# Performance work log

Hardware: AMD Instinct MI355X
Metric: run time of the kernel (lower is better)

Reference implementation:

```python
import jax, jax.numpy as jnp
import numpy as np

N, D_MODEL, NUM_HEAD = 2, 256, 8
HI, WI = 40, 40
MAX_DIS = 7
WS = 2 * MAX_DIS + 1          # 15
HD = D_MODEL // NUM_HEAD      # 32
T = HD ** 0.5
NEG = 1e8                     # fp32 mask value used by the torch module


def setup_inputs() -> dict:
    key = jax.random.key(0)
    ks = jax.random.split(key, 10)
    s = 0.02
    f = lambda i, shape: jax.random.normal(ks[i], shape, jnp.float32)
    return dict(
        q=f(0, (N, D_MODEL, HI, WI)),
        k=f(1, (N, D_MODEL, HI, WI)),
        v=f(2, (N, D_MODEL, HI, WI)),
        Wq=f(3, (D_MODEL, D_MODEL)) * s, bq=jnp.zeros((D_MODEL,), jnp.float32),
        Wk=f(4, (D_MODEL, D_MODEL)) * s, bk=jnp.zeros((D_MODEL,), jnp.float32),
        Wv=f(5, (D_MODEL, D_MODEL)) * s, bv=jnp.zeros((D_MODEL,), jnp.float32),
        rel_k_w=f(6, (NUM_HEAD, WS * WS, HD)) * s,      # grouped 1x1 conv weight
        rel_k_b=jnp.zeros((NUM_HEAD, WS * WS), jnp.float32),
        rel_v=f(7, (NUM_HEAD, HD, WS * WS)) * s,        # nn.Parameter (zeros in torch; random here to exercise math)
        Wp=f(8, (D_MODEL, D_MODEL)) * s, bp=jnp.zeros((D_MODEL,), jnp.float32),
    )


def _geometry(h, w):
    # Static (numpy) index/mask construction matching compute_mask().
    qy = np.repeat(np.arange(h), w)
    qx = np.tile(np.arange(w), h)
    dy = qy[None, :] - qy[:, None]          # key - query, [hw, hw]
    dx = qx[None, :] - qx[:, None]
    valid = (np.abs(dy) <= MAX_DIS) & (np.abs(dx) <= MAX_DIS)
    widx = (np.clip(dy + MAX_DIS, 0, WS - 1) * WS + np.clip(dx + MAX_DIS, 0, WS - 1))
    offs = np.arange(-MAX_DIS, MAX_DIS + 1)
    dyo = np.repeat(offs, WS)               # [ws*ws] row-major window order (dy*WS+dx)
    dxo = np.tile(offs, WS)
    ky = qy[:, None] + dyo[None, :]         # [hw, ws*ws]
    kx = qx[:, None] + dxo[None, :]
    in_img = (ky >= 0) & (ky < h) & (kx >= 0) & (kx < w)
    jidx = np.clip(ky, 0, h - 1) * w + np.clip(kx, 0, w - 1)
    return (jnp.asarray(valid), jnp.asarray(widx), jnp.asarray(in_img), jnp.asarray(jidx))


def reference(q, k, v, Wq, bq, Wk, bk, Wv, bv, rel_k_w, rel_k_b, rel_v, Wp, bp):
    n, c, h, w = q.shape
    hw = h * w
    nh, hd = NUM_HEAD, c // NUM_HEAD

    def proj(x, Wt, b):  # 1x1 conv == per-pixel linear
        return jnp.einsum('oc,ncp->nop', Wt, x.reshape(n, c, hw)) + b[None, :, None]

    qf = proj(q, Wq, bq)
    kf = proj(k, Wk, bk)
    vf = proj(v, Wv, bv)

    qh = qf.reshape(n, nh, hd, hw)
    kh = kf.reshape(n, nh, hd, hw)
    vh = vf.reshape(n, nh, hd, hw)

    # grouped 1x1 conv: per-head linear from hd channels to ws*ws (computed BEFORE q/T)
    rel = jnp.einsum('hwd,nhdp->nhpw', rel_k_w, qh) + rel_k_b[None, :, None, :]  # [n,nh,hw,ws2]

    qh = qh / T
    qk = jnp.einsum('nhdi,nhdj->nhij', qh, kh)   # [n,nh,hw,hw]

    valid, widx, in_img, jidx = _geometry(h, w)

    # --- 'global' path: dense hw x hw, non-local keys masked with -1e8, local keys get rel bias ---
    rel_dense = jnp.take_along_axis(rel, widx[None, None], axis=3)   # [n,nh,hw,hw]
    global_logits = jnp.where(valid[None, None], qk + rel_dense, qk - NEG)
    global_attn = jax.nn.softmax(global_logits, axis=-1)
    agg_value = jnp.einsum('nhij,nhdj->inhd', global_attn, vh).reshape(hw, n, c)

    # --- local path: gather ws*ws window per query; out-of-image keys are -1e8 (pad value), rel added everywhere ---
    gathered = jnp.take_along_axis(qk, jidx[None, None], axis=3)     # [n,nh,hw,ws2]
    local_logits = jnp.where(in_img[None, None], gathered, -NEG) + rel
    local_attn = jax.nn.softmax(local_logits, axis=-1)
    agg_bias = jnp.einsum('nhiw,hdw->inhd', local_attn, rel_v).reshape(hw, n, c)

    out = (agg_value + agg_bias) @ Wp.T + bp    # nn.Linear, output [hw, n, c]
    return out, local_attn
```

## Files before the change

### kernel.cpp

```cpp
#include <hip/hip_runtime.h>
#include <hip/hip_bf16.h>

#define HW    1600
#define NB    2
#define NHEAD 8
#define HD    32
#define WS2   225
#define WDIM  40
#define CDIM  256
#define PROJ  819200
#define RELW  240
#define RELSTR 248
#define TSC   5.656854249492381f

typedef __attribute__((ext_vector_type(8))) short short8;
typedef __attribute__((ext_vector_type(4))) float floatx4;

static __device__ __forceinline__ float bu2f(short u) {
    return __uint_as_float(((unsigned)(unsigned short)u) << 16);
}
static __device__ __forceinline__ short f2bu(float f) {
    __hip_bfloat16 h = __float2bfloat16(f);
    short s; __builtin_memcpy(&s, &h, 2); return s;
}
static __device__ __forceinline__ unsigned pk2(short a, short b) {
    return (unsigned)(unsigned short)a | ((unsigned)(unsigned short)b << 16);
}
static __device__ __forceinline__ float ldf(const void* p, size_t i, bool f32) {
    return f32 ? ((const float*)p)[i] : __bfloat162float(((const __hip_bfloat16*)p)[i]);
}
static __device__ __forceinline__ void st_out(void* p, size_t i, float v, bool f32) {
    if (f32) ((float*)p)[i] = v;
    else     ((__hip_bfloat16*)p)[i] = __float2bfloat16(v);
}
static __device__ __forceinline__ short8 ld8bf(const void* p, size_t i, bool f32) {
    if (!f32) return *(const short8*)((const __hip_bfloat16*)p + i);
    const float* f = (const float*)p + i;
    short8 r;
    #pragma unroll
    for (int t = 0; t < 8; ++t) r[t] = f2bu(f[t]);
    return r;
}
static __device__ __forceinline__ void ld8f(const void* p, size_t i, bool f32, float* o) {
    if (f32) {
        const float* f = (const float*)p + i;
        #pragma unroll
        for (int t = 0; t < 8; ++t) o[t] = f[t];
    } else {
        short8 s = *(const short8*)((const __hip_bfloat16*)p + i);
        #pragma unroll
        for (int t = 0; t < 8; ++t) o[t] = bu2f(s[t]);
    }
}

__global__ __launch_bounds__(64) void detect_kernel(const void* qv, int* flag) {
    const __hip_bfloat16* qb = (const __hip_bfloat16*)qv;
    int bad = 0;
    for (int i = threadIdx.x; i < 4096; i += 64) {
        float v = __bfloat162float(qb[i]);
        if (!(v > -1e6f && v < 1e6f)) bad = 1;
    }
    bad = (__any(bad) ? 1 : 0);
    if (threadIdx.x == 0) *flag = bad;
}

__global__ __launch_bounds__(256) void relvT_kernel(const void* __restrict__ relv,
                                                    const int* __restrict__ flag,
                                                    __hip_bfloat16* __restrict__ relvT) {
    const bool f32 = (*flag != 0);
    const int h = blockIdx.x;
    for (int idx = threadIdx.x; idx < WS2 * HD; idx += 256) {
        const int w = idx >> 5, d = idx & 31;
        relvT[(size_t)h * WS2 * HD + idx] =
            __float2bfloat16(ldf(relv, ((size_t)h * HD + d) * WS2 + w, f32));
    }
}

__global__ __launch_bounds__(256) void proj_fused(
    const void* __restrict__ xq, const void* __restrict__ xk, const void* __restrict__ xv,
    const void* __restrict__ Wq, const void* __restrict__ bq,
    const void* __restrict__ Wk, const void* __restrict__ bk,
    const void* __restrict__ Wv, const void* __restrict__ bv,
    const int* __restrict__ flag,
    __hip_bfloat16* __restrict__ qs, __hip_bfloat16* __restrict__ ks,
    __hip_bfloat16* __restrict__ vs)
{
    __shared__ short xt[32][264];
    const bool f32 = (*flag != 0);
    const int m0 = blockIdx.x * 32;
    const int n  = blockIdx.y;
    const int t  = blockIdx.z;
    const void *x, *W, *bias; __hip_bfloat16* dst; float scale;
    if (t == 0)      { x = xq; W = Wq; bias = bq; dst = qs; scale = 0.17677669529663687f; }
    else if (t == 1) { x = xk; W = Wk; bias = bk; dst = ks; scale = 1.f; }
    else             { x = xv; W = Wv; bias = bv; dst = vs; scale = 1.f; }

    {
        const int c = threadIdx.x;
        const size_t xb = ((size_t)n * CDIM + c) * HW + m0;
        if (f32) {
            const float* xr = (const float*)x + xb;
            #pragma unroll
            for (int g = 0; g < 8; ++g) {
                float4 f = *(const float4*)(xr + g * 4);
                xt[g*4+0][c] = f2bu(f.x); xt[g*4+1][c] = f2bu(f.y);
                xt[g*4+2][c] = f2bu(f.z); xt[g*4+3][c] = f2bu(f.w);
            }
        } else {
            const __hip_bfloat16* xr = (const __hip_bfloat16*)x + xb;
            #pragma unroll
            for (int g = 0; g < 4; ++g) {
                short8 s = *(const short8*)(xr + g * 8);
                #pragma unroll
                for (int u = 0; u < 8; ++u) xt[g*8+u][c] = s[u];
            }
        }
    }
    __syncthreads();

    const int wave = threadIdx.x >> 6, lane = threadIdx.x & 63;
    const int m = lane & 15, qd = lane >> 4;

    short8 A[2][8];
    #pragma unroll
    for (int mt = 0; mt < 2; ++mt)
        #pragma unroll
        for (int k = 0; k < 8; ++k)
            A[mt][k] = *(const short8*)(&xt[mt*16 + m][k*32 + qd*8]);

    #pragma unroll
    for (int og = 0; og < 4; ++og) {
        const int o0 = (wave * 4 + og) * 16;
        short8 B[8];
        #pragma unroll
        for (int k = 0; k < 8; ++k)
            B[k] = ld8bf(W, (size_t)(o0 + m) * CDIM + k*32 + qd*8, f32);
        floatx4 acc0 = {0,0,0,0}, acc1 = {0,0,0,0};
        #pragma unroll
        for (int k = 0; k < 8; ++k) {
            acc0 = __builtin_amdgcn_mfma_f32_16x16x32_bf16(A[0][k], B[k], acc0, 0, 0, 0);
            acc1 = __builtin_amdgcn_mfma_f32_16x16x32_bf16(A[1][k], B[k], acc1, 0, 0, 0);
        }
        const int o = o0 + (lane & 15), h = o >> 5, d = o & 31;
        const float bv_ = ldf(bias, (size_t)o, f32);
        #pragma unroll
        for (int rg = 0; rg < 4; ++rg) {
            const int p = m0 + (lane >> 4) * 4 + rg;
            dst[((size_t)(n*NHEAD + h)*HW + p)*HD + d]      = __float2bfloat16((acc0[rg] + bv_) * scale);
            dst[((size_t)(n*NHEAD + h)*HW + p + 16)*HD + d] = __float2bfloat16((acc1[rg] + bv_) * scale);
        }
    }
}

__global__ __launch_bounds__(256) void rel_gemm(
    const __hip_bfloat16* __restrict__ qs, const void* __restrict__ rkw,
    const void* __restrict__ rkb, const int* __restrict__ flag,
    __hip_bfloat16* __restrict__ rel)
{
    const bool f32 = (*flag != 0);
    const int wave = threadIdx.x >> 6, lane = threadIdx.x & 63;
    const int i0 = blockIdx.x * 64;
    const int nh_ = blockIdx.y;
    const int h = nh_ & 7;
    const int m = lane & 15, qd = lane >> 4;

    short8 A[4];
    #pragma unroll
    for (int it = 0; it < 4; ++it)
        A[it] = *(const short8*)(qs + ((size_t)nh_ * HW + i0 + it*16 + m) * HD + qd*8);

    for (int wt = wave; wt < 15; wt += 4) {
        const int w0 = wt * 16;
        const int wl = min(w0 + m, WS2 - 1);
        short8 B = ld8bf(rkw, ((size_t)h * WS2 + wl) * HD + qd*8, f32);
        const int wcol = w0 + (lane & 15);
        const float rb_ = (wcol < WS2) ? ldf(rkb, (size_t)h * WS2 + wcol, f32) : 0.f;
        #pragma unroll
        for (int it = 0; it < 4; ++it) {
            floatx4 acc = {0,0,0,0};
            acc = __builtin_amdgcn_mfma_f32_16x16x32_bf16(A[it], B, acc, 0, 0, 0);
            if (wcol < WS2) {
                #pragma unroll
                for (int rg = 0; rg < 4; ++rg) {
                    const int i = i0 + it*16 + (lane >> 4)*4 + rg;
                    rel[((size_t)nh_ * HW + i) * RELW + wcol] =
                        __float2bfloat16(acc[rg] * TSC + rb_);
                }
            }
        }
    }
}

#define SP_OFF    0
#define R2_OFF    15616
#define R1_OFF    24064
#define SMAX_OFF  39680
#define SSUM_OFF  39936
#define SMEM_SZ   40192

__global__ __launch_bounds__(256) void attn_mfma(
    const __hip_bfloat16* __restrict__ qs, const __hip_bfloat16* __restrict__ ks,
    const __hip_bfloat16* __restrict__ vs,
    const __hip_bfloat16* __restrict__ rel,
    const __hip_bfloat16* __restrict__ relvT,
    const int* __restrict__ flag,
    __hip_bfloat16* __restrict__ agg,
    void* __restrict__ dout)
{
    __shared__ __align__(16) char smem[SMEM_SZ];
    short* sP   = (short*)(smem + SP_OFF);
    short* sRel = (short*)(smem + R2_OFF);
    short* sPw  = (short*)(smem + R2_OFF);
    short* sB   = (short*)(smem + R1_OFF);
    float* sOh  = (float*)(smem + R1_OFF);
    float* sMax = (float*)(smem + SMAX_OFF);
    float* sSum = (float*)(smem + SSUM_OFF);

    const bool f32 = (*flag != 0);
    const int tid = threadIdx.x;
    const int wave = tid >> 6, lane = tid & 63;
    const int m = lane & 15, quad = lane >> 4;
    const int y = blockIdx.x / 3, tile3 = blockIdx.x % 3;
    const int x0 = (tile3 == 0) ? 0 : (tile3 == 1) ? 16 : 24;
    const int wlo = (tile3 == 2) ? 8 : 0;
    const int nh_ = blockIdx.y;
    const int h = nh_ & 7, n = nh_ >> 3;
    const size_t qb = (size_t)nh_ * HW;
    const size_t qrow0 = qb + (size_t)y * WDIM + x0;

    for (int idx = tid; idx < 480; idx += 256) {
        const int row = idx / 30, c8 = (idx - row * 30) * 8;
        short8 v = *(const short8*)((const short*)rel + (qrow0 + row) * RELW + c8);
        *(short8*)(sRel + row * RELSTR + c8) = v;
    }
    const short8 afrag = *(const short8*)((const short*)qs + (qrow0 + m) * HD + quad * 8);
    __syncthreads();

    float L[8][4];
    #pragma unroll
    for (int j = 0; j < 8; ++j)
        #pragma unroll
        for (int rg = 0; rg < 4; ++rg) L[j][rg] = -1e30f;

    #pragma unroll
    for (int j = 0; j < 8; ++j) {
        const int t = wave + 4 * j;
        if (t < 30) {
            const int r = t >> 1, c0_ = (t & 1) << 4;
            const int cc = c0_ + m;
            const int ky = y + r - 7, kx = x0 - 7 + cc;
            const int gky = min(max(ky, 0), WDIM - 1), gkx = min(max(kx, 0), WDIM - 1);
            const short8 bfrag = *(const short8*)((const short*)ks + (qb + (size_t)gky * WDIM + gkx) * HD + quad * 8);
            floatx4 s4 = {0.f, 0.f, 0.f, 0.f};
            s4 = __builtin_amdgcn_mfma_f32_16x16x32_bf16(afrag, bfrag, s4, 0, 0, 0);
            const bool inimg = ((unsigned)ky < (unsigned)WDIM) && ((unsigned)kx < (unsigned)WDIM);
            #pragma unroll
            for (int rg = 0; rg < 4; ++rg) {
                const int qm = quad * 4 + rg;
                const int dx7 = cc - qm;
                if (inimg && (unsigned)dx7 < 15u)
                    L[j][rg] = s4[rg] + bu2f(sRel[qm * RELSTR + r * 15 + dx7]);
            }
        }
    }

    float mx[4];
    #pragma unroll
    for (int rg = 0; rg < 4; ++rg) {
        mx[rg] = L[0][rg];
        #pragma unroll
        for (int j = 1; j < 8; ++j) mx[rg] = fmaxf(mx[rg], L[j][rg]);
        #pragma unroll
        for (int off = 1; off <= 8; off <<= 1) mx[rg] = fmaxf(mx[rg], __shfl_xor(mx[rg], off));
    }
    if (m == 0) {
        #pragma unroll
        for (int rg = 0; rg < 4; ++rg) sMax[(quad * 4 + rg) * 4 + wave] = mx[rg];
    }
    __syncthreads();
    float M4[4], sm[4];
    #pragma unroll
    for (int rg = 0; rg < 4; ++rg) {
        const float4 v = *(const float4*)&sMax[(quad * 4 + rg) * 4];
        M4[rg] = fmaxf(fmaxf(v.x, v.y), fmaxf(v.z, v.w));
        sm[rg] = 0.f;
    }
    #pragma unroll
    for (int j = 0; j < 8; ++j)
        #pragma unroll
        for (int rg = 0; rg < 4; ++rg) { L[j][rg] = expf(L[j][rg] - M4[rg]); sm[rg] += L[j][rg]; }
    #pragma unroll
    for (int rg = 0; rg < 4; ++rg)
        #pragma unroll
        for (int off = 1; off <= 8; off <<= 1) sm[rg] += __shfl_xor(sm[rg], off);
    if (m == 0) {
        #pragma unroll
        for (int rg = 0; rg < 4; ++rg) sSum[(quad * 4 + rg) * 4 + wave] = sm[rg];
    }
    __syncthreads();
    float inv4[4];
    #pragma unroll
    for (int rg = 0; rg < 4; ++rg) {
        const float4 v = *(const float4*)&sSum[(quad * 4 + rg) * 4];
        inv4[rg] = 1.f / (v.x + v.y + v.z + v.w);
    }

    for (int e = tid; e < 16 * 39; e += 256) {
        const int row = e / 39, c = 225 + (e - row * 39);
        sPw[row * 264 + c] = 0;
    }

    #pragma unroll
    for (int j = 0; j < 8; ++j) {
        const int t = wave + 4 * j;
        if (t < 30) {
            const int r = t >> 1, cc = ((t & 1) << 4) + m;
            #pragma unroll
            for (int rg = 0; rg < 4; ++rg) {
                const int qm = quad * 4 + rg;
                const short pb = f2bu(L[j][rg] * inv4[rg]);
                sP[qm * 488 + r * 32 + cc] = pb;
                const int dx7 = cc - qm;
                if ((unsigned)dx7 < 15u) sPw[qm * 264 + r * 15 + dx7] = pb;
            }
        }
    }
    __syncthreads();

    #pragma unroll
    for (int rr = 0; rr < 4; ++rr) {
        const int qm = wave * 4 + rr;
        if (qm >= wlo) {
            const size_t obase = (size_t)PROJ + (qrow0 + qm) * WS2;
            #pragma unroll
            for (int c = 0; c < 4; ++c) {
                const int col = lane + 64 * c;
                if (col < WS2) st_out(dout, obase + col, bu2f(sPw[qm * 264 + col]), f32);
            }
        }
    }

    for (int half = 0; half < 2; ++half) {
        __syncthreads();
        const int h16 = half << 4;
        {
            unsigned* dstw = (unsigned*)sB;
            for (int p = tid; p < 240; p += 256) {
                const int kk0 = 2 * p;
                const int r = kk0 >> 5, c = kk0 & 31;
                const int gky = min(max(y + r - 7, 0), WDIM - 1);
                const int gkx0 = min(max(x0 - 7 + c, 0), WDIM - 1);
                const int gkx1 = min(max(x0 - 7 + c + 1, 0), WDIM - 1);
                const short* v0 = (const short*)vs + (qb + (size_t)gky * WDIM + gkx0) * HD + h16;
                const short* v1 = (const short*)vs + (qb + (size_t)gky * WDIM + gkx1) * HD + h16;
                const short8 a0 = *(const short8*)v0, b0 = *(const short8*)v1;
                const short8 a1 = *(const short8*)(v0 + 8), b1 = *(const short8*)(v1 + 8);
                #pragma unroll
                for (int dd = 0; dd < 8; ++dd) dstw[dd * 244 + p] = pk2(a0[dd], b0[dd]);
                #pragma unroll
                for (int dd = 0; dd < 8; ++dd) dstw[(dd + 8) * 244 + p] = pk2(a1[dd], b1[dd]);
            }
        }
        __syncthreads();
        floatx4 acc = {0.f, 0.f, 0.f, 0.f};
        for (int u = wave; u < 15; u += 4) {
            const short8 Af = *(const short8*)(sP + m * 488 + u * 32 + quad * 8);
            const short8 Bf = *(const short8*)(sB + m * 488 + u * 32 + quad * 8);
            acc = __builtin_amdgcn_mfma_f32_16x16x32_bf16(Af, Bf, acc, 0, 0, 0);
        }
        __syncthreads();
        {
            unsigned* dstw = (unsigned*)sB;
            for (int p = tid; p < 132; p += 256) {
                const int w0 = 2 * p;
                short8 a0 = {0,0,0,0,0,0,0,0}, a1 = a0, b0 = a0, b1 = a0;
                if (w0 < WS2) {
                    const short* rp = (const short*)relvT + ((size_t)h * WS2 + w0) * HD + h16;
                    a0 = *(const short8*)rp; a1 = *(const short8*)(rp + 8);
                }
                if (w0 + 1 < WS2) {
                    const short* rp = (const short*)relvT + ((size_t)h * WS2 + w0 + 1) * HD + h16;
                    b0 = *(const short8*)rp; b1 = *(const short8*)(rp + 8);
                }
                #pragma unroll
                for (int dd = 0; dd < 8; ++dd) dstw[dd * 132 + p] = pk2(a0[dd], b0[dd]);
                #pragma unroll
                for (int dd = 0; dd < 8; ++dd) dstw[(dd + 8) * 132 + p] = pk2(a1[dd], b1[dd]);
            }
        }
        __syncthreads();
        for (int u = wave; u < 8; u += 4) {
            const short8 Af = *(const short8*)(sPw + m * 264 + u * 32 + quad * 8);
            const short8 Bf = *(const short8*)(sB + m * 264 + u * 32 + quad * 8);
            acc = __builtin_amdgcn_mfma_f32_16x16x32_bf16(Af, Bf, acc, 0, 0, 0);
        }
        __syncthreads();
        #pragma unroll
        for (int rg = 0; rg < 4; ++rg)
            sOh[wave * 256 + (quad * 4 + rg) * 16 + m] = acc[rg];
        __syncthreads();
        {
            const int qq = tid >> 4, dd = tid & 15;
            const float s = sOh[tid] + sOh[256 + tid] + sOh[512 + tid] + sOh[768 + tid];
            if (qq >= wlo) {
                const size_t i = (size_t)y * WDIM + x0 + qq;
                agg[(i * NB + n) * CDIM + h * HD + h16 + dd] = __float2bfloat16(s);
            }
        }
    }
}

__global__ __launch_bounds__(256) void attn_fallback(
    const __hip_bfloat16* __restrict__ qs, const __hip_bfloat16* __restrict__ ks,
    const __hip_bfloat16* __restrict__ vs,
    const __hip_bfloat16* __restrict__ relvT,
    const void* __restrict__ rkw, const void* __restrict__ rkb,
    const int* __restrict__ flag,
    __hip_bfloat16* __restrict__ agg,
    void* __restrict__ dout)
{
    __shared__ float sL[4][240];

    const bool f32 = (*flag != 0);
    const int wave = threadIdx.x >> 6, lane = threadIdx.x & 63;
    const int qidx = blockIdx.x * 4 + wave;
    const int i = qidx % HW, nh_ = qidx / HW;
    const int h = nh_ & (NHEAD - 1), n = nh_ >> 3;
    const int y = i / WDIM, x = i - y * WDIM;

    const int w16 = lane >> 2, qq = lane & 3;
    float q8[8];
    {
        short8 qv = *(const short8*)(qs + (size_t)qidx * HD + qq * 8);
        #pragma unroll
        for (int t = 0; t < 8; ++t) q8[t] = bu2f(qv[t]);
    }

    const int kxu = x + w16 - 7;
    const bool vw = (w16 < 15);
    for (int r = 0; r < 15; ++r) {
        const int ky = y + r - 7;
        const int widx = r * 15 + w16;
        const bool vimg = vw && ((unsigned)ky < WDIM) && ((unsigned)kxu < WDIM);
        float part = 0.f;
        if (vimg) {
            short8 kv = *(const short8*)(ks + ((size_t)nh_ * HW + ky * WDIM + kxu) * HD + qq * 8);
            float r8[8];
            ld8f(rkw, ((size_t)h * WS2 + widx) * HD + qq * 8, f32, r8);
            #pragma unroll
            for (int t = 0; t < 8; ++t) part += q8[t] * (bu2f(kv[t]) + TSC * r8[t]);
        }
        part += __shfl_xor(part, 1);
        part += __shfl_xor(part, 2);
        if (qq == 0) {
            float lg = -1e30f;
            if (vimg) lg = part + ldf(rkb, (size_t)h * WS2 + widx, f32);
            sL[wave][vw ? widx : (225 + r)] = lg;
        }
    }

    float lg[4];
    float mx = -1e30f;
    #pragma unroll
    for (int c = 0; c < 4; ++c) {
        const int w_ = lane + 64 * c;
        lg[c] = (w_ < 240) ? sL[wave][w_] : -1e30f;
        mx = fmaxf(mx, lg[c]);
    }
    #pragma unroll
    for (int off = 32; off > 0; off >>= 1) mx = fmaxf(mx, __shfl_xor(mx, off));
    float s = 0.f;
    #pragma unroll
    for (int c = 0; c < 4; ++c) { lg[c] = expf(lg[c] - mx); s += lg[c]; }
    #pragma unroll
    for (int off = 32; off > 0; off >>= 1) s += __shfl_xor(s, off);
    const float inv = (s > 0.f) ? (1.0f / s) : 0.f;
    #pragma unroll
    for (int c = 0; c < 4; ++c) {
        const int w_ = lane + 64 * c;
        if (w_ < WS2) {
            const float a = lg[c] * inv;
            sL[wave][w_] = a;
            st_out(dout, (size_t)PROJ + (size_t)qidx * WS2 + w_, a, f32);
        }
    }

    float o8[8] = {0.f, 0.f, 0.f, 0.f, 0.f, 0.f, 0.f, 0.f};
    if (vw) {
        for (int r = 0; r < 15; ++r) {
            const int widx = r * 15 + w16;
            const int kyc = min(max(y + r - 7, 0), WDIM - 1);
            const int kxc = min(max(kxu, 0), WDIM - 1);
            const float P = sL[wave][widx];
            short8 vv = *(const short8*)(vs + ((size_t)nh_ * HW + kyc * WDIM + kxc) * HD + qq * 8);
            short8 rv = *(const short8*)(relvT + ((size_t)h * WS2 + widx) * HD + qq * 8);
            #pragma unroll
            for (int t = 0; t < 8; ++t) o8[t] += P * (bu2f(vv[t]) + bu2f(rv[t]));
        }
    }
    #pragma unroll
    for (int off = 4; off <= 32; off <<= 1)
        #pragma unroll
        for (int t = 0; t < 8; ++t) o8[t] += __shfl_xor(o8[t], off);
    if (lane < 4) {
        short8 tmp;
        #pragma unroll
        for (int t = 0; t < 8; ++t) tmp[t] = f2bu(o8[t]);
        *(short8*)(agg + ((size_t)i * NB + n) * CDIM + h * HD + qq * 8) = tmp;
    }
}

__global__ __launch_bounds__(256) void out_mfma(
    const __hip_bfloat16* __restrict__ agg, const void* __restrict__ Wp,
    const void* __restrict__ bp, const int* __restrict__ flag,
    void* __restrict__ dout)
{
    const bool f32 = (*flag != 0);
    const int wave = threadIdx.x >> 6, lane = threadIdx.x & 63;
    const int tile = blockIdx.x * 4 + wave;
    const int rb0 = tile & ~15;
    const int o0 = (tile & 15) << 4;
    const int m = lane & 15, qd = lane >> 4;

    const __hip_bfloat16* arow = agg + (size_t)(rb0 + m) * CDIM + qd * 8;
    const size_t bidx = (size_t)(o0 + m) * CDIM + qd * 8;

    floatx4 acc = {0.f, 0.f, 0.f, 0.f};
    #pragma unroll
    for (int k = 0; k < 8; ++k) {
        short8 a = *(const short8*)(arow + k * 32);
        short8 b = ld8bf(Wp, bidx + k * 32, f32);
        acc = __builtin_amdgcn_mfma_f32_16x16x32_bf16(a, b, acc, 0, 0, 0);
    }
    const int o = o0 + (lane & 15);
    const float bv_ = ldf(bp, (size_t)o, f32);
    #pragma unroll
    for (int rg = 0; rg < 4; ++rg) {
        const int rb = rb0 + (lane >> 4) * 4 + rg;
        st_out(dout, (size_t)rb * CDIM + o, acc[rg] + bv_, f32);
    }
}

extern "C" void kernel_launch(void* const* d_in, const int* in_sizes, int n_in,
                              void* d_out, int out_size, void* d_ws, size_t ws_size,
                              hipStream_t stream)
{
    const void* q   = d_in[0];
    const void* k   = d_in[1];
    const void* v   = d_in[2];
    const void* Wq  = d_in[3];
    const void* bq  = d_in[4];
    const void* Wk  = d_in[5];
    const void* bk  = d_in[6];
    const void* Wv  = d_in[7];
    const void* bv  = d_in[8];
    const void* rkw = d_in[9];
    const void* rkb = d_in[10];
    const void* rlv = d_in[11];
    const void* Wp  = d_in[12];
    const void* bp  = d_in[13];

    char* wsb = (char*)d_ws;
    int* flag = (int*)wsb;
    __hip_bfloat16* relvT = (__hip_bfloat16*)(wsb + 64);
    __hip_bfloat16* qs    = (__hip_bfloat16*)(wsb + 64 + 115200);
    __hip_bfloat16* ks    = qs + PROJ;
    __hip_bfloat16* vs    = ks + PROJ;
    __hip_bfloat16* agg   = vs + PROJ;
    __hip_bfloat16* rel   = agg + PROJ;
    const size_t need = 64 + 115200 + (size_t)4 * PROJ * 2 + (size_t)NB * NHEAD * HW * RELW * 2;
    const bool userel = (ws_size >= need);

    detect_kernel<<<1, 64, 0, stream>>>(q, flag);
    relvT_kernel<<<8, 256, 0, stream>>>(rlv, flag, relvT);
    proj_fused<<<dim3(50, 2, 3), 256, 0, stream>>>(q, k, v, Wq, bq, Wk, bk, Wv, bv,
                                                   flag, qs, ks, vs);
    if (userel) {
        rel_gemm<<<dim3(25, 16), 256, 0, stream>>>(qs, rkw, rkb, flag, rel);
        attn_mfma<<<dim3(120, 16), 256, 0, stream>>>(qs, ks, vs, rel, relvT, flag, agg, d_out);
    } else {
        attn_fallback<<<6400, 256, 0, stream>>>(qs, ks, vs, relvT, rkw, rkb, flag, agg, d_out);
    }
    out_mfma<<<800, 256, 0, stream>>>(agg, Wp, bp, flag, d_out);
}
```

Measured before the change: 183.8 us.

## Fuse rel GEMM into attention, merge prep kernels, widen output GEMM tiles

The relative-key GEMM now runs inside the attention kernel: each block computes its own 16x225 rel tile with MFMA straight into shared memory, so the global rel buffer round trip and the separate rel_gemm launch go away. The detect and relvT transpose kernels become one prep kernel, cutting a launch. The output projection computes two 16-column tiles per wave, halving the grid and reusing each A fragment. The fallback attention path is removed, and the per-block rel computation adds a little extra work and a sync inside attention.

```diff
diff --git a/kernel.cpp b/kernel.cpp
--- a/kernel.cpp
+++ b/kernel.cpp
@@ -9,7 +9,6 @@
 #define WDIM  40
 #define CDIM  256
 #define PROJ  819200
-#define RELW  240
 #define RELSTR 248
 #define TSC   5.656854249492381f
 
@@ -41,33 +40,24 @@
     for (int t = 0; t < 8; ++t) r[t] = f2bu(f[t]);
     return r;
 }
-static __device__ __forceinline__ void ld8f(const void* p, size_t i, bool f32, float* o) {
-    if (f32) {
-        const float* f = (const float*)p + i;
-        #pragma unroll
-        for (int t = 0; t < 8; ++t) o[t] = f[t];
-    } else {
-        short8 s = *(const short8*)((const __hip_bfloat16*)p + i);
-        #pragma unroll
-        for (int t = 0; t < 8; ++t) o[t] = bu2f(s[t]);
-    }
-}
-
-__global__ __launch_bounds__(64) void detect_kernel(const void* qv, int* flag) {
-    const __hip_bfloat16* qb = (const __hip_bfloat16*)qv;
+
+__global__ __launch_bounds__(256) void prep_kernel(const void* __restrict__ q,
+                                                   const void* __restrict__ relv,
+                                                   int* __restrict__ flag,
+                                                   __hip_bfloat16* __restrict__ relvT) {
+    __shared__ int sbad;
+    if (threadIdx.x == 0) sbad = 0;
+    __syncthreads();
     int bad = 0;
-    for (int i = threadIdx.x; i < 4096; i += 64) {
+    const __hip_bfloat16* qb = (const __hip_bfloat16*)q;
+    for (int i = threadIdx.x; i < 4096; i += 256) {
         float v = __bfloat162float(qb[i]);
         if (!(v > -1e6f && v < 1e6f)) bad = 1;
     }
-    bad = (__any(bad) ? 1 : 0);
-    if (threadIdx.x == 0) *flag = bad;
-}
-
-__global__ __launch_bounds__(256) void relvT_kernel(const void* __restrict__ relv,
-                                                    const int* __restrict__ flag,
-                                                    __hip_bfloat16* __restrict__ relvT) {
-    const bool f32 = (*flag != 0);
+    if (bad) sbad = 1;
+    __syncthreads();
+    const bool f32 = (sbad != 0);
+    if (blockIdx.x == 0 && threadIdx.x == 0) *flag = sbad;
     const int h = blockIdx.x;
     for (int idx = threadIdx.x; idx < WS2 * HD; idx += 256) {
         const int w = idx >> 5, d = idx & 31;
@@ -152,56 +142,18 @@
     }
 }
 
-__global__ __launch_bounds__(256) void rel_gemm(
-    const __hip_bfloat16* __restrict__ qs, const void* __restrict__ rkw,
-    const void* __restrict__ rkb, const int* __restrict__ flag,
-    __hip_bfloat16* __restrict__ rel)
-{
-    const bool f32 = (*flag != 0);
-    const int wave = threadIdx.x >> 6, lane = threadIdx.x & 63;
-    const int i0 = blockIdx.x * 64;
-    const int nh_ = blockIdx.y;
-    const int h = nh_ & 7;
-    const int m = lane & 15, qd = lane >> 4;
-
-    short8 A[4];
-    #pragma unroll
-    for (int it = 0; it < 4; ++it)
-        A[it] = *(const short8*)(qs + ((size_t)nh_ * HW + i0 + it*16 + m) * HD + qd*8);
-
-    for (int wt = wave; wt < 15; wt += 4) {
-        const int w0 = wt * 16;
-        const int wl = min(w0 + m, WS2 - 1);
-        short8 B = ld8bf(rkw, ((size_t)h * WS2 + wl) * HD + qd*8, f32);
-        const int wcol = w0 + (lane & 15);
-        const float rb_ = (wcol < WS2) ? ldf(rkb, (size_t)h * WS2 + wcol, f32) : 0.f;
-        #pragma unroll
-        for (int it = 0; it < 4; ++it) {
-            floatx4 acc = {0,0,0,0};
-            acc = __builtin_amdgcn_mfma_f32_16x16x32_bf16(A[it], B, acc, 0, 0, 0);
-            if (wcol < WS2) {
-                #pragma unroll
-                for (int rg = 0; rg < 4; ++rg) {
-                    const int i = i0 + it*16 + (lane >> 4)*4 + rg;
-                    rel[((size_t)nh_ * HW + i) * RELW + wcol] =
-                        __float2bfloat16(acc[rg] * TSC + rb_);
-                }
-            }
-        }
-    }
-}
-
 #define SP_OFF    0
 #define R2_OFF    15616
 #define R1_OFF    24064
 #define SMAX_OFF  39680
 #define SSUM_OFF  39936
-#define SMEM_SZ   40192
+#define SRKB_OFF  40192
+#define SMEM_SZ   40672
 
 __global__ __launch_bounds__(256) void attn_mfma(
     const __hip_bfloat16* __restrict__ qs, const __hip_bfloat16* __restrict__ ks,
     const __hip_bfloat16* __restrict__ vs,
-    const __hip_bfloat16* __restrict__ rel,
+    const void* __restrict__ rkw, const void* __restrict__ rkb,
     const __hip_bfloat16* __restrict__ relvT,
     const int* __restrict__ flag,
     __hip_bfloat16* __restrict__ agg,
@@ -215,6 +167,7 @@
     float* sOh  = (float*)(smem + R1_OFF);
     float* sMax = (float*)(smem + SMAX_OFF);
     float* sSum = (float*)(smem + SSUM_OFF);
+    short* sRkb = (short*)(smem + SRKB_OFF);
 
     const bool f32 = (*flag != 0);
     const int tid = threadIdx.x;
@@ -228,12 +181,25 @@
     const size_t qb = (size_t)nh_ * HW;
     const size_t qrow0 = qb + (size_t)y * WDIM + x0;
 
-    for (int idx = tid; idx < 480; idx += 256) {
-        const int row = idx / 30, c8 = (idx - row * 30) * 8;
-        short8 v = *(const short8*)((const short*)rel + (qrow0 + row) * RELW + c8);
-        *(short8*)(sRel + row * RELSTR + c8) = v;
-    }
+    for (int wv = tid; wv < 240; wv += 256)
+        sRkb[wv] = (wv < WS2) ? f2bu(ldf(rkb, (size_t)h * WS2 + wv, f32)) : (short)0;
     const short8 afrag = *(const short8*)((const short*)qs + (qrow0 + m) * HD + quad * 8);
+    __syncthreads();
+
+    for (int wt = wave; wt < 15; wt += 4) {
+        const int w0 = wt * 16;
+        const int wl = min(w0 + m, WS2 - 1);
+        short8 B = ld8bf(rkw, ((size_t)h * WS2 + wl) * HD + quad * 8, f32);
+        floatx4 acc = {0.f, 0.f, 0.f, 0.f};
+        acc = __builtin_amdgcn_mfma_f32_16x16x32_bf16(afrag, B, acc, 0, 0, 0);
+        const int wcol = w0 + m;
+        if (wcol < WS2) {
+            const float rb_ = bu2f(sRkb[wcol]);
+            #pragma unroll
+            for (int rg = 0; rg < 4; ++rg)
+                sRel[(quad * 4 + rg) * RELSTR + wcol] = f2bu(acc[rg] * TSC + rb_);
+        }
+    }
     __syncthreads();
 
     float L[8][4];
@@ -410,106 +376,6 @@
     }
 }
 
-__global__ __launch_bounds__(256) void attn_fallback(
-    const __hip_bfloat16* __restrict__ qs, const __hip_bfloat16* __restrict__ ks,
-    const __hip_bfloat16* __restrict__ vs,
-    const __hip_bfloat16* __restrict__ relvT,
-    const void* __restrict__ rkw, const void* __restrict__ rkb,
-    const int* __restrict__ flag,
-    __hip_bfloat16* __restrict__ agg,
-    void* __restrict__ dout)
-{
-    __shared__ float sL[4][240];
-
-    const bool f32 = (*flag != 0);
-    const int wave = threadIdx.x >> 6, lane = threadIdx.x & 63;
-    const int qidx = blockIdx.x * 4 + wave;
-    const int i = qidx % HW, nh_ = qidx / HW;
-    const int h = nh_ & (NHEAD - 1), n = nh_ >> 3;
-    const int y = i / WDIM, x = i - y * WDIM;
-
-    const int w16 = lane >> 2, qq = lane & 3;
-    float q8[8];
-    {
-        short8 qv = *(const short8*)(qs + (size_t)qidx * HD + qq * 8);
-        #pragma unroll
-        for (int t = 0; t < 8; ++t) q8[t] = bu2f(qv[t]);
-    }
-
-    const int kxu = x + w16 - 7;
-    const bool vw = (w16 < 15);
-    for (int r = 0; r < 15; ++r) {
-        const int ky = y + r - 7;
-        const int widx = r * 15 + w16;
-        const bool vimg = vw && ((unsigned)ky < WDIM) && ((unsigned)kxu < WDIM);
-        float part = 0.f;
-        if (vimg) {
-            short8 kv = *(const short8*)(ks + ((size_t)nh_ * HW + ky * WDIM + kxu) * HD + qq * 8);
-            float r8[8];
-            ld8f(rkw, ((size_t)h * WS2 + widx) * HD + qq * 8, f32, r8);
-            #pragma unroll
-            for (int t = 0; t < 8; ++t) part += q8[t] * (bu2f(kv[t]) + TSC * r8[t]);
-        }
-        part += __shfl_xor(part, 1);
-        part += __shfl_xor(part, 2);
-        if (qq == 0) {
-            float lg = -1e30f;
-            if (vimg) lg = part + ldf(rkb, (size_t)h * WS2 + widx, f32);
-            sL[wave][vw ? widx : (225 + r)] = lg;
-        }
-    }
-
-    float lg[4];
-    float mx = -1e30f;
-    #pragma unroll
-    for (int c = 0; c < 4; ++c) {
-        const int w_ = lane + 64 * c;
-        lg[c] = (w_ < 240) ? sL[wave][w_] : -1e30f;
-        mx = fmaxf(mx, lg[c]);
-    }
-    #pragma unroll
-    for (int off = 32; off > 0; off >>= 1) mx = fmaxf(mx, __shfl_xor(mx, off));
-    float s = 0.f;
-    #pragma unroll
-    for (int c = 0; c < 4; ++c) { lg[c] = expf(lg[c] - mx); s += lg[c]; }
-    #pragma unroll
-    for (int off = 32; off > 0; off >>= 1) s += __shfl_xor(s, off);
-    const float inv = (s > 0.f) ? (1.0f / s) : 0.f;
-    #pragma unroll
-    for (int c = 0; c < 4; ++c) {
-        const int w_ = lane + 64 * c;
-        if (w_ < WS2) {
-            const float a = lg[c] * inv;
-            sL[wave][w_] = a;
-            st_out(dout, (size_t)PROJ + (size_t)qidx * WS2 + w_, a, f32);
-        }
-    }
-
-    float o8[8] = {0.f, 0.f, 0.f, 0.f, 0.f, 0.f, 0.f, 0.f};
-    if (vw) {
-        for (int r = 0; r < 15; ++r) {
-            const int widx = r * 15 + w16;
-            const int kyc = min(max(y + r - 7, 0), WDIM - 1);
-            const int kxc = min(max(kxu, 0), WDIM - 1);
-            const float P = sL[wave][widx];
-            short8 vv = *(const short8*)(vs + ((size_t)nh_ * HW + kyc * WDIM + kxc) * HD + qq * 8);
-            short8 rv = *(const short8*)(relvT + ((size_t)h * WS2 + widx) * HD + qq * 8);
-            #pragma unroll
-            for (int t = 0; t < 8; ++t) o8[t] += P * (bu2f(vv[t]) + bu2f(rv[t]));
-        }
-    }
-    #pragma unroll
-    for (int off = 4; off <= 32; off <<= 1)
-        #pragma unroll
-        for (int t = 0; t < 8; ++t) o8[t] += __shfl_xor(o8[t], off);
-    if (lane < 4) {
-        short8 tmp;
-        #pragma unroll
-        for (int t = 0; t < 8; ++t) tmp[t] = f2bu(o8[t]);
-        *(short8*)(agg + ((size_t)i * NB + n) * CDIM + h * HD + qq * 8) = tmp;
-    }
-}
-
 __global__ __launch_bounds__(256) void out_mfma(
     const __hip_bfloat16* __restrict__ agg, const void* __restrict__ Wp,
     const void* __restrict__ bp, const int* __restrict__ flag,
@@ -517,27 +383,30 @@
 {
     const bool f32 = (*flag != 0);
     const int wave = threadIdx.x >> 6, lane = threadIdx.x & 63;
-    const int tile = blockIdx.x * 4 + wave;
-    const int rb0 = tile & ~15;
-    const int o0 = (tile & 15) << 4;
+    const int t2 = blockIdx.x * 4 + wave;
+    const int rb0 = (t2 >> 3) << 4;
+    const int o0 = (t2 & 7) << 5;
     const int m = lane & 15, qd = lane >> 4;
 
     const __hip_bfloat16* arow = agg + (size_t)(rb0 + m) * CDIM + qd * 8;
-    const size_t bidx = (size_t)(o0 + m) * CDIM + qd * 8;
-
-    floatx4 acc = {0.f, 0.f, 0.f, 0.f};
+
+    floatx4 acc0 = {0.f, 0.f, 0.f, 0.f}, acc1 = {0.f, 0.f, 0.f, 0.f};
     #pragma unroll
     for (int k = 0; k < 8; ++k) {
-        short8 a = *(const short8*)(arow + k * 32);
-        short8 b = ld8bf(Wp, bidx + k * 32, f32);
-        acc = __builtin_amdgcn_mfma_f32_16x16x32_bf16(a, b, acc, 0, 0, 0);
-    }
-    const int o = o0 + (lane & 15);
-    const float bv_ = ldf(bp, (size_t)o, f32);
+        short8 a  = *(const short8*)(arow + k * 32);
+        short8 b0 = ld8bf(Wp, (size_t)(o0 + m) * CDIM + k * 32 + qd * 8, f32);
+        short8 b1 = ld8bf(Wp, (size_t)(o0 + 16 + m) * CDIM + k * 32 + qd * 8, f32);
+        acc0 = __builtin_amdgcn_mfma_f32_16x16x32_bf16(a, b0, acc0, 0, 0, 0);
+        acc1 = __builtin_amdgcn_mfma_f32_16x16x32_bf16(a, b1, acc1, 0, 0, 0);
+    }
+    const int oa = o0 + (lane & 15), ob = oa + 16;
+    const float ba_ = ldf(bp, (size_t)oa, f32);
+    const float bb_ = ldf(bp, (size_t)ob, f32);
     #pragma unroll
     for (int rg = 0; rg < 4; ++rg) {
         const int rb = rb0 + (lane >> 4) * 4 + rg;
-        st_out(dout, (size_t)rb * CDIM + o, acc[rg] + bv_, f32);
+        st_out(dout, (size_t)rb * CDIM + oa, acc0[rg] + ba_, f32);
+        st_out(dout, (size_t)rb * CDIM + ob, acc1[rg] + bb_, f32);
     }
 }
 
@@ -567,19 +436,10 @@
     __hip_bfloat16* ks    = qs + PROJ;
     __hip_bfloat16* vs    = ks + PROJ;
     __hip_bfloat16* agg   = vs + PROJ;
-    __hip_bfloat16* rel   = agg + PROJ;
-    const size_t need = 64 + 115200 + (size_t)4 * PROJ * 2 + (size_t)NB * NHEAD * HW * RELW * 2;
-    const bool userel = (ws_size >= need);
-
-    detect_kernel<<<1, 64, 0, stream>>>(q, flag);
-    relvT_kernel<<<8, 256, 0, stream>>>(rlv, flag, relvT);
+
+    prep_kernel<<<8, 256, 0, stream>>>(q, rlv, flag, relvT);
     proj_fused<<<dim3(50, 2, 3), 256, 0, stream>>>(q, k, v, Wq, bq, Wk, bk, Wv, bv,
                                                    flag, qs, ks, vs);
-    if (userel) {
-        rel_gemm<<<dim3(25, 16), 256, 0, stream>>>(qs, rkw, rkb, flag, rel);
-        attn_mfma<<<dim3(120, 16), 256, 0, stream>>>(qs, ks, vs, rel, relvT, flag, agg, d_out);
-    } else {
-        attn_fallback<<<6400, 256, 0, stream>>>(qs, ks, vs, relvT, rkw, rkb, flag, agg, d_out);
-    }
-    out_mfma<<<800, 256, 0, stream>>>(agg, Wp, bp, flag, d_out);
-}
+    attn_mfma<<<dim3(120, 16), 256, 0, stream>>>(qs, ks, vs, rkw, rkb, relvT, flag, agg, d_out);
+    out_mfma<<<400, 256, 0, stream>>>(agg, Wp, bp, flag, d_out);
+}
```

Measured after the change: 169.1 us. 8.0% less time.
